# Optimization experiments

Hardware: AMD Instinct MI355X
Metric: run time of the kernel (lower is better)

The kernel has to match this reference:

```python
import jax, jax.numpy as jnp
import numpy as np

BETA = 0.25
CODEBOOK_SIZE = 1024
EMBED_DIM = 256


def setup_inputs() -> dict:
    key = jax.random.key(0)
    k1, k2 = jax.random.split(key)
    z_e = jax.random.normal(k1, (32, EMBED_DIM, 32, 32), dtype=jnp.float32)
    lim = 1.0 / CODEBOOK_SIZE
    emb_weight = jax.random.uniform(k2, (CODEBOOK_SIZE, EMBED_DIM),
                                    dtype=jnp.float32, minval=-lim, maxval=lim)
    return {"z_e": z_e, "emb_weight": emb_weight}


def reference(z_e, emb_weight):
    B, D, Gh, Gw = z_e.shape
    # (B, D, Gh, Gw) -> (N, D), N = B*Gh*Gw
    z_flat = jnp.transpose(z_e, (0, 2, 3, 1)).reshape(-1, D)

    # squared distances via ||z||^2 + ||e||^2 - 2 z.e
    z2 = jnp.sum(z_flat * z_flat, axis=1, keepdims=True)          # (N, 1)
    e2 = jnp.sum(emb_weight * emb_weight, axis=1)[None, :]        # (1, K)
    ze = jnp.einsum('nd,kd->nk', z_flat, emb_weight)              # (N, K)
    dist = z2 + e2 - 2.0 * ze

    idx_flat = jnp.argmin(dist, axis=1)                            # (N,)
    z_q_flat = emb_weight[idx_flat]                                # (N, D)

    sg = jax.lax.stop_gradient
    codebook_loss = jnp.mean((z_q_flat - sg(z_flat)) ** 2)
    commit_loss = jnp.mean((z_flat - sg(z_q_flat)) ** 2)
    vq_loss = codebook_loss + BETA * commit_loss

    # straight-through estimator
    z_q_st_flat = z_flat + sg(z_q_flat - z_flat)

    z_q_st = jnp.transpose(z_q_st_flat.reshape(B, Gh, Gw, D), (0, 3, 1, 2))
    idx = idx_flat.reshape(B, Gh, Gw)
    return z_q_st, idx, vq_loss
```

## Files before the change

### kernel.cpp

```cpp
#include <hip/hip_runtime.h>
#include <hip/hip_fp16.h>

#define MARGIN 6e-4f
#define RCAP 48

typedef __attribute__((ext_vector_type(8))) _Float16 half8;
typedef __attribute__((ext_vector_type(4))) float f32x4;

__device__ __forceinline__ unsigned short f2h(float x) {
    __half h = __float2half(x);
    return *reinterpret_cast<unsigned short*>(&h);
}
__device__ __forceinline__ void gload16(const void* g, void* l) {
    __builtin_amdgcn_global_load_lds(
        (const __attribute__((address_space(1))) void*)g,
        (__attribute__((address_space(3))) void*)l, 16, 0, 0);
}

__global__ __launch_bounds__(256) void k_prep_e(const float* __restrict__ e,
                                                float* __restrict__ e2,
                                                unsigned short* __restrict__ eh,
                                                int* __restrict__ rowCnt,
                                                float* __restrict__ lossAcc,
                                                int* __restrict__ doneCnt) {
    const int bi = blockIdx.x;
    const int t  = threadIdx.x;
    if (bi < 4) {
        int k = bi * 256 + t;
        const float4* p = (const float4*)(e + (size_t)k * 256);
        float s = 0.f;
#pragma unroll 4
        for (int c = 0; c < 64; ++c) {
            float4 v = p[c];
            s = fmaf(v.x, v.x, s); s = fmaf(v.y, v.y, s);
            s = fmaf(v.z, v.z, s); s = fmaf(v.w, v.w, s);
        }
        e2[k] = s;
    } else {
        int bb = bi - 4;
        int k0 = bb * 64;
#pragma unroll 4
        for (int i = 0; i < 16; ++i) {
            int flat = i * 256 + t;
            int row = flat >> 6, ch = flat & 63;
            int slab = ch >> 4, s8p = (ch >> 1) & 7, half = ch & 1;
            int s8 = s8p ^ (row & 7);
            int d  = slab * 64 + s8 * 8 + half * 4;
            float4 v = *(const float4*)(e + (size_t)(k0 + row) * 256 + d);
            uint2 ph = { (unsigned)f2h(v.x) | ((unsigned)f2h(v.y) << 16),
                         (unsigned)f2h(v.z) | ((unsigned)f2h(v.w) << 16) };
            size_t off = (size_t)(k0 + row) * 256 + slab * 64 + s8p * 8 + half * 4;
            *(uint2*)(eh + off) = ph;
        }
        if (bb == 0 && t == 0) { lossAcc[0] = 0.f; doneCnt[0] = 0; }
#pragma unroll
        for (int j = 0; j < 8; ++j)
            rowCnt[bb * 2048 + j * 256 + t] = 0;
    }
}

__global__ __launch_bounds__(512) void k_score(
        const float* __restrict__ z,
        const unsigned short* __restrict__ eh,
        const float* __restrict__ e2,
        float* __restrict__ z2,
        int* __restrict__ rowCnt, uint2* __restrict__ rowCand) {
    __shared__ unsigned short lds[32768];
    float* tile = (float*)&lds[16384];

    const int t    = threadIdx.x;
    const int lane = t & 63;
    const int w    = t >> 6;
    const int wr   = w >> 1;
    const int wc   = w & 1;
    const int c    = lane & 15;
    const int kq   = lane >> 4;
    const int n0   = blockIdx.x * 64;
    const int b    = n0 >> 10;
    const int nl0  = n0 & 1023;

    {
        float zs = 0.f;
        const int prow = t & 63;
        const int uu0  = (t >> 6) * 4;
        for (int ch = 0; ch < 4; ++ch) {
            const int d0 = ch * 64;
            __syncthreads();
#pragma unroll
            for (int i = 0; i < 2; ++i) {
                int flat = i * 512 + t;
                int dd = flat >> 4, q = flat & 15;
                float4 v = *(const float4*)(z + (size_t)b * 262144 +
                                            (size_t)(d0 + dd) * 1024 + nl0 + q * 4);
                int j0 = q * 4, sx = dd & 31;
                tile[dd * 64 + ((j0 + 0) ^ sx)] = v.x;
                tile[dd * 64 + ((j0 + 1) ^ sx)] = v.y;
                tile[dd * 64 + ((j0 + 2) ^ sx)] = v.z;
                tile[dd * 64 + ((j0 + 3) ^ sx)] = v.w;
            }
            __syncthreads();
            if (t < 64) {
#pragma unroll 16
                for (int dd = 0; dd < 64; ++dd) {
                    float v = tile[dd * 64 + (t ^ (dd & 31))];
                    zs = fmaf(v, v, zs);
                }
            }
#pragma unroll
            for (int u = uu0; u < uu0 + 4; ++u) {
                int dlo = u * 2;
                float a0 = tile[dlo * 64 + (prow ^ (dlo & 31))];
                float a1 = tile[(dlo + 1) * 64 + (prow ^ ((dlo + 1) & 31))];
                unsigned int pk = (unsigned)f2h(a0) | ((unsigned)f2h(a1) << 16);
                int g = u >> 2, w32 = u & 3;
                *(unsigned int*)&lds[prow * 256 + d0 +
                                     ((g ^ (prow & 7)) * 8) + w32 * 2] = pk;
            }
        }
        __syncthreads();
        if (t < 64) z2[n0 + t] = zs;
    }

#define STAGE_B(S, BUF)                                                      \
    do {                                                                     \
        int kc_ = (S) >> 2, dg_ = (S) & 3;                                   \
        _Pragma("unroll")                                                    \
        for (int p = 0; p < 2; ++p) {                                        \
            int slot = p * 512 + t;                                          \
            int code = slot >> 3, sg = slot & 7;                             \
            gload16(eh + (size_t)(kc_ * 128 + code) * 256 + dg_ * 64 + sg * 8, \
                    &lds[16384 + (BUF) * 8192 + (p * 512 + w * 64) * 8]);    \
        }                                                                    \
    } while (0)

    f32x4 acc[4];
#pragma unroll
    for (int cf = 0; cf < 4; ++cf) acc[cf] = (f32x4){0.f, 0.f, 0.f, 0.f};
    float m_run[4] = { 3.4e38f, 3.4e38f, 3.4e38f, 3.4e38f };

    const int rl = wr * 16 + c;
    STAGE_B(0, 0);
    __syncthreads();

    for (int s = 0; s < 32; ++s) {
        if (s < 31) STAGE_B(s + 1, (s + 1) & 1);
        {
            const int dg = s & 3;
            const unsigned short* Bb = &lds[16384 + (s & 1) * 8192];
#pragma unroll
            for (int ks = 0; ks < 2; ++ks) {
                int wo = ks * 4 + kq;
                half8 a = *(const half8*)&lds[rl * 256 + dg * 64 +
                                              (wo ^ (rl & 7)) * 8];
                half8 bfr[4];
#pragma unroll
                for (int cf = 0; cf < 4; ++cf) {
                    int cl = wc * 64 + cf * 16 + c;
                    bfr[cf] = *(const half8*)&Bb[cl * 64 + (wo ^ (cl & 7)) * 8];
                }
#pragma unroll
                for (int cf = 0; cf < 4; ++cf)
                    acc[cf] = __builtin_amdgcn_mfma_f32_16x16x32_f16(
                        a, bfr[cf], acc[cf], 0, 0, 0);
            }
        }
        if ((s & 3) == 3) {
            const int kc = s >> 2;
            float e2r[4];
#pragma unroll
            for (int cf = 0; cf < 4; ++cf)
                e2r[cf] = e2[kc * 128 + wc * 64 + cf * 16 + c];
            float mnew[4];
#pragma unroll
            for (int reg = 0; reg < 4; ++reg) {
                float mm = 3.4e38f;
#pragma unroll
                for (int cf = 0; cf < 4; ++cf)
                    mm = fminf(mm, fmaf(-2.f, acc[cf][reg], e2r[cf]));
                mnew[reg] = mm;
            }
#pragma unroll
            for (int m = 1; m < 16; m <<= 1)
#pragma unroll
                for (int reg = 0; reg < 4; ++reg)
                    mnew[reg] = fminf(mnew[reg], __shfl_xor(mnew[reg], m, 64));
#pragma unroll
            for (int reg = 0; reg < 4; ++reg)
                mnew[reg] = fminf(mnew[reg], m_run[reg]);
#pragma unroll
            for (int cf = 0; cf < 4; ++cf)
#pragma unroll
                for (int reg = 0; reg < 4; ++reg) {
                    float sv = fmaf(-2.f, acc[cf][reg], e2r[cf]);
                    if (sv <= mnew[reg] + MARGIN) {
                        int n = n0 + wr * 16 + kq * 4 + reg;
                        int k = kc * 128 + wc * 64 + cf * 16 + c;
                        int pos = atomicAdd(&rowCnt[n], 1);
                        if (pos < RCAP) {
                            uint2 cd; cd.x = (unsigned)k;
                            cd.y = __float_as_uint(sv);
                            rowCand[n * RCAP + pos] = cd;
                        }
                    }
                }
#pragma unroll
            for (int reg = 0; reg < 4; ++reg) m_run[reg] = mnew[reg];
#pragma unroll
            for (int cf = 0; cf < 4; ++cf) acc[cf] = (f32x4){0.f, 0.f, 0.f, 0.f};
        }
        __syncthreads();
    }
#undef STAGE_B
}

__global__ __launch_bounds__(256) void k_select(
        const float* __restrict__ z, const float* __restrict__ e,
        const float* __restrict__ z2a, const float* __restrict__ e2,
        const int* __restrict__ rowCnt, const uint2* __restrict__ rowCand,
        float* __restrict__ outIdx, int* __restrict__ wsIdx) {
    __shared__ float zstage[4][256];
    const int t = threadIdx.x, lane = t & 63, w = t >> 6;
    const int wid = blockIdx.x * 4 + w;
    for (int rr = 0; rr < 8; ++rr) {
        const int n = wid * 8 + rr;
        const int cnt = rowCnt[n];
        const float* zrow = z + (size_t)(n >> 10) * 262144 + (n & 1023);
        unsigned long long key = 0xFFFFFFFFFFFFFFFFULL;
        if (cnt <= RCAP) {
            float s = 3.4e38f;
            int   k = 0;
            if (lane < cnt) {
                uint2 cd = rowCand[n * RCAP + lane];
                k = (int)cd.x;
                s = __uint_as_float(cd.y);
            }
            float gmin = s;
#pragma unroll
            for (int m = 1; m < 64; m <<= 1)
                gmin = fminf(gmin, __shfl_xor(gmin, m, 64));
            bool surv = (lane < cnt) && (s <= gmin + MARGIN);
            unsigned long long bal = __ballot(surv);
            if (__popcll(bal) == 1) {
                if (surv) { outIdx[n] = (float)k; wsIdx[n] = k; }
                continue;
            }
#pragma unroll
            for (int j = 0; j < 4; ++j)
                zstage[w][lane + 64 * j] = zrow[(size_t)(lane + 64 * j) * 1024];
            if (surv) {
                const float* er = e + (size_t)k * 256;
                float ze = 0.f;
#pragma unroll 8
                for (int d = 0; d < 256; ++d)
                    ze = fmaf(zstage[w][d], er[d], ze);
                float t1 = z2a[n] + e2[k];
                float dist = fmaf(-2.f, ze, t1);
                key = ((unsigned long long)__float_as_uint(dist) << 32) |
                      (unsigned int)k;
            }
        } else {
#pragma unroll
            for (int j = 0; j < 4; ++j)
                zstage[w][lane + 64 * j] = zrow[(size_t)(lane + 64 * j) * 1024];
            const float z2r = z2a[n];
            for (int j = 0; j < 16; ++j) {
                int k = lane * 16 + j;
                const float* er = e + (size_t)k * 256;
                float ze = 0.f;
#pragma unroll 8
                for (int d = 0; d < 256; ++d)
                    ze = fmaf(zstage[w][d], er[d], ze);
                float t1 = z2r + e2[k];
                float dist = fmaf(-2.f, ze, t1);
                unsigned long long kk =
                    ((unsigned long long)__float_as_uint(dist) << 32) |
                    (unsigned int)k;
                if (kk < key) key = kk;
            }
        }
#pragma unroll
        for (int m = 1; m < 64; m <<= 1) {
            unsigned long long o = __shfl_xor(key, m, 64);
            if (o < key) key = o;
        }
        if (lane == 0) {
            int k = (int)(unsigned int)(key & 0xFFFFFFFFULL);
            outIdx[n] = (float)k;
            wsIdx[n]  = k;
        }
    }
}

__global__ __launch_bounds__(256) void k_epilogue(const float* __restrict__ z,
                                                  const float* __restrict__ e,
                                                  const int* __restrict__ wsIdx,
                                                  float* __restrict__ outZ,
                                                  float* __restrict__ lossAcc,
                                                  int* __restrict__ doneCnt,
                                                  float* __restrict__ outLoss) {
    __shared__ float zqT[8][1024];
    __shared__ int idxL[1024];
    __shared__ float wsum[4];
    const int t  = threadIdx.x;
    const int b  = blockIdx.x >> 5;
    const int dg = blockIdx.x & 31;
    const size_t zb = (size_t)b * 262144 + (size_t)(dg * 8) * 1024;

    float4 zreg[8];
#pragma unroll
    for (int i = 0; i < 8; ++i) {
        int flat = i * 256 + t;
        int dl = flat >> 8, q = flat & 255;
        zreg[i] = *(const float4*)(z + zb + (size_t)dl * 1024 + q * 4);
    }

#pragma unroll
    for (int c = 0; c < 4; ++c)
        idxL[c * 256 + t] = wsIdx[b * 1024 + c * 256 + t];
    __syncthreads();

#pragma unroll
    for (int c = 0; c < 4; ++c) {
        int nl = c * 256 + t;
        const float* er = e + (size_t)idxL[nl] * 256 + dg * 8;
        float4 v0 = *(const float4*)er;
        float4 v1 = *(const float4*)(er + 4);
        zqT[0][nl] = v0.x; zqT[1][nl] = v0.y;
        zqT[2][nl] = v0.z; zqT[3][nl] = v0.w;
        zqT[4][nl] = v1.x; zqT[5][nl] = v1.y;
        zqT[6][nl] = v1.z; zqT[7][nl] = v1.w;
    }
    __syncthreads();

    float s = 0.f;
#pragma unroll
    for (int i = 0; i < 8; ++i) {
        int flat = i * 256 + t;
        int dl = flat >> 8, q = flat & 255;
        float4 z4 = zreg[i];
        float4 q4 = *(const float4*)&zqT[dl][q * 4];
        float4 o; float df;
        df = q4.x - z4.x; s = fmaf(df, df, s); o.x = z4.x + df;
        df = q4.y - z4.y; s = fmaf(df, df, s); o.y = z4.y + df;
        df = q4.z - z4.z; s = fmaf(df, df, s); o.z = z4.z + df;
        df = q4.w - z4.w; s = fmaf(df, df, s); o.w = z4.w + df;
        *(float4*)(outZ + zb + (size_t)dl * 1024 + q * 4) = o;
    }

#pragma unroll
    for (int off = 32; off > 0; off >>= 1) s += __shfl_down(s, off, 64);
    if ((t & 63) == 0) wsum[t >> 6] = s;
    __syncthreads();
    if (t == 0) {
        float bs = ((wsum[0] + wsum[1]) + wsum[2]) + wsum[3];
        atomicAdd(lossAcc, bs);
        __threadfence();
        int tk = atomicAdd(doneCnt, 1);
        if (tk == 1023) {
            float L = atomicAdd(lossAcc, 0.0f);
            float m = L * (1.0f / 8388608.0f);
            outLoss[0] = m + 0.25f * m;
        }
    }
}

extern "C" void kernel_launch(void* const* d_in, const int* in_sizes, int n_in,
                              void* d_out, int out_size, void* d_ws, size_t ws_size,
                              hipStream_t stream) {
    const float* z = (const float*)d_in[0];
    const float* e = (const float*)d_in[1];
    float* out     = (float*)d_out;
    float* outIdx  = out + 8388608;
    float* outLoss = out + 8421376;

    float* z2      = (float*)d_ws;
    float* e2      = z2 + 32768;
    float* lossAcc = e2 + 1024;
    int*   doneCnt = (int*)(lossAcc + 64);
    int*   rowCnt  = doneCnt + 64;
    int*   wsIdx   = rowCnt + 32768;
    uintptr_t p = (uintptr_t)(wsIdx + 32768);
    p = (p + 255) & ~(uintptr_t)255;
    uint2* rowCand = (uint2*)p;
    unsigned short* eh = (unsigned short*)(rowCand + 32768 * RCAP);

    k_prep_e<<<20, 256, 0, stream>>>(e, e2, eh, rowCnt, lossAcc, doneCnt);
    k_score<<<512, 512, 0, stream>>>(z, eh, e2, z2, rowCnt, rowCand);
    k_select<<<1024, 256, 0, stream>>>(z, e, z2, e2, rowCnt, rowCand,
                                       outIdx, wsIdx);
    k_epilogue<<<1024, 256, 0, stream>>>(z, e, wsIdx, out, lossAcc,
                                         doneCnt, outLoss);
}
```

Baseline: 163.9 us.

## Fuse candidate selection into scoring kernel and restructure epilogue gather

Folds the k_select pass into the tail of k_score, so each block resolves the argmin for its own 64 rows right after scoring. This removes a kernel launch and the global round-trip of z2, and e2 and z2 are now kept in LDS. The epilogue is remapped to 512 blocks that gather codebook rows straight into registers (16 dims by 4 consecutive positions per thread) instead of staging through a transposed LDS tile. The cost is that selection now depends on same-block visibility of atomics and candidates (guarded by a fence and a barrier), and it runs at k_score's occupancy.

```diff
diff --git a/kernel.cpp b/kernel.cpp
--- a/kernel.cpp
+++ b/kernel.cpp
@@ -61,11 +61,15 @@
 
 __global__ __launch_bounds__(512) void k_score(
         const float* __restrict__ z,
+        const float* __restrict__ e,
         const unsigned short* __restrict__ eh,
         const float* __restrict__ e2,
-        float* __restrict__ z2,
-        int* __restrict__ rowCnt, uint2* __restrict__ rowCand) {
+        int* __restrict__ rowCnt, uint2* __restrict__ rowCand,
+        float* __restrict__ outIdx, int* __restrict__ wsIdx) {
     __shared__ unsigned short lds[32768];
+    __shared__ float e2L[1024];
+    __shared__ float z2L[64];
+
     float* tile = (float*)&lds[16384];
 
     const int t    = threadIdx.x;
@@ -79,6 +83,9 @@
     const int b    = n0 >> 10;
     const int nl0  = n0 & 1023;
 
+    e2L[t]       = e2[t];
+    e2L[t + 512] = e2[t + 512];
+
     {
         float zs = 0.f;
         const int prow = t & 63;
@@ -118,7 +125,7 @@
             }
         }
         __syncthreads();
-        if (t < 64) z2[n0 + t] = zs;
+        if (t < 64) z2L[t] = zs;
     }
 
 #define STAGE_B(S, BUF)                                                      \
@@ -169,7 +176,7 @@
             float e2r[4];
 #pragma unroll
             for (int cf = 0; cf < 4; ++cf)
-                e2r[cf] = e2[kc * 128 + wc * 64 + cf * 16 + c];
+                e2r[cf] = e2L[kc * 128 + wc * 64 + cf * 16 + c];
             float mnew[4];
 #pragma unroll
             for (int reg = 0; reg < 4; ++reg) {
@@ -211,82 +218,80 @@
         __syncthreads();
     }
 #undef STAGE_B
-}
-
-__global__ __launch_bounds__(256) void k_select(
-        const float* __restrict__ z, const float* __restrict__ e,
-        const float* __restrict__ z2a, const float* __restrict__ e2,
-        const int* __restrict__ rowCnt, const uint2* __restrict__ rowCand,
-        float* __restrict__ outIdx, int* __restrict__ wsIdx) {
-    __shared__ float zstage[4][256];
-    const int t = threadIdx.x, lane = t & 63, w = t >> 6;
-    const int wid = blockIdx.x * 4 + w;
-    for (int rr = 0; rr < 8; ++rr) {
-        const int n = wid * 8 + rr;
-        const int cnt = rowCnt[n];
-        const float* zrow = z + (size_t)(n >> 10) * 262144 + (n & 1023);
-        unsigned long long key = 0xFFFFFFFFFFFFFFFFULL;
-        if (cnt <= RCAP) {
-            float s = 3.4e38f;
-            int   k = 0;
-            if (lane < cnt) {
-                uint2 cd = rowCand[n * RCAP + lane];
-                k = (int)cd.x;
-                s = __uint_as_float(cd.y);
-            }
-            float gmin = s;
-#pragma unroll
-            for (int m = 1; m < 64; m <<= 1)
-                gmin = fminf(gmin, __shfl_xor(gmin, m, 64));
-            bool surv = (lane < cnt) && (s <= gmin + MARGIN);
-            unsigned long long bal = __ballot(surv);
-            if (__popcll(bal) == 1) {
-                if (surv) { outIdx[n] = (float)k; wsIdx[n] = k; }
-                continue;
-            }
-#pragma unroll
-            for (int j = 0; j < 4; ++j)
-                zstage[w][lane + 64 * j] = zrow[(size_t)(lane + 64 * j) * 1024];
-            if (surv) {
-                const float* er = e + (size_t)k * 256;
-                float ze = 0.f;
+
+    asm volatile("s_waitcnt vmcnt(0)" ::: "memory");
+    __threadfence();
+    __syncthreads();
+    {
+        float* zst = (float*)&lds[16384 + w * 512];
+        for (int rr = 0; rr < 8; ++rr) {
+            const int n = n0 + w * 8 + rr;
+            const int rloc = w * 8 + rr;
+            const int cnt = rowCnt[n];
+            const float* zrow = z + (size_t)b * 262144 + (n & 1023);
+            unsigned long long key = 0xFFFFFFFFFFFFFFFFULL;
+            if (cnt <= RCAP) {
+                float sc = 3.4e38f;
+                int   k = 0;
+                if (lane < cnt) {
+                    uint2 cd = rowCand[n * RCAP + lane];
+                    k = (int)cd.x;
+                    sc = __uint_as_float(cd.y);
+                }
+                float gmin = sc;
+#pragma unroll
+                for (int m = 1; m < 64; m <<= 1)
+                    gmin = fminf(gmin, __shfl_xor(gmin, m, 64));
+                bool surv = (lane < cnt) && (sc <= gmin + MARGIN);
+                unsigned long long bal = __ballot(surv);
+                if (__popcll(bal) == 1) {
+                    if (surv) { outIdx[n] = (float)k; wsIdx[n] = k; }
+                    continue;
+                }
+#pragma unroll
+                for (int j = 0; j < 4; ++j)
+                    zst[lane + 64 * j] = zrow[(size_t)(lane + 64 * j) * 1024];
+                if (surv) {
+                    const float* erk = e + (size_t)k * 256;
+                    float ze = 0.f;
 #pragma unroll 8
-                for (int d = 0; d < 256; ++d)
-                    ze = fmaf(zstage[w][d], er[d], ze);
-                float t1 = z2a[n] + e2[k];
-                float dist = fmaf(-2.f, ze, t1);
-                key = ((unsigned long long)__float_as_uint(dist) << 32) |
-                      (unsigned int)k;
-            }
-        } else {
-#pragma unroll
-            for (int j = 0; j < 4; ++j)
-                zstage[w][lane + 64 * j] = zrow[(size_t)(lane + 64 * j) * 1024];
-            const float z2r = z2a[n];
-            for (int j = 0; j < 16; ++j) {
-                int k = lane * 16 + j;
-                const float* er = e + (size_t)k * 256;
-                float ze = 0.f;
+                    for (int d = 0; d < 256; ++d)
+                        ze = fmaf(zst[d], erk[d], ze);
+                    float t1 = z2L[rloc] + e2L[k];
+                    float dist = fmaf(-2.f, ze, t1);
+                    key = ((unsigned long long)__float_as_uint(dist) << 32) |
+                          (unsigned int)k;
+                }
+            } else {
+#pragma unroll
+                for (int j = 0; j < 4; ++j)
+                    zst[lane + 64 * j] = zrow[(size_t)(lane + 64 * j) * 1024];
+                const float z2r = z2L[rloc];
+                for (int j = 0; j < 16; ++j) {
+                    int k = lane * 16 + j;
+                    const float* erk = e + (size_t)k * 256;
+                    float ze = 0.f;
 #pragma unroll 8
-                for (int d = 0; d < 256; ++d)
-                    ze = fmaf(zstage[w][d], er[d], ze);
-                float t1 = z2r + e2[k];
-                float dist = fmaf(-2.f, ze, t1);
-                unsigned long long kk =
-                    ((unsigned long long)__float_as_uint(dist) << 32) |
-                    (unsigned int)k;
-                if (kk < key) key = kk;
-            }
-        }
-#pragma unroll
-        for (int m = 1; m < 64; m <<= 1) {
-            unsigned long long o = __shfl_xor(key, m, 64);
-            if (o < key) key = o;
-        }
-        if (lane == 0) {
-            int k = (int)(unsigned int)(key & 0xFFFFFFFFULL);
-            outIdx[n] = (float)k;
-            wsIdx[n]  = k;
+                    for (int d = 0; d < 256; ++d)
+                        ze = fmaf(zst[d], erk[d], ze);
+                    float t1 = z2r + e2L[k];
+                    float dist = fmaf(-2.f, ze, t1);
+                    unsigned long long kk =
+                        ((unsigned long long)__float_as_uint(dist) << 32) |
+                        (unsigned int)k;
+                    if (kk < key) key = kk;
+                }
+            }
+#pragma unroll
+            for (int m = 1; m < 64; m <<= 1) {
+                unsigned long long o = __shfl_xor(key, m, 64);
+                if (o < key) key = o;
+            }
+            if (lane == 0) {
+                int k = (int)(unsigned int)(key & 0xFFFFFFFFULL);
+                outIdx[n] = (float)k;
+                wsIdx[n]  = k;
+            }
         }
     }
 }
@@ -298,53 +303,38 @@
                                                   float* __restrict__ lossAcc,
                                                   int* __restrict__ doneCnt,
                                                   float* __restrict__ outLoss) {
-    __shared__ float zqT[8][1024];
-    __shared__ int idxL[1024];
     __shared__ float wsum[4];
     const int t  = threadIdx.x;
-    const int b  = blockIdx.x >> 5;
-    const int dg = blockIdx.x & 31;
-    const size_t zb = (size_t)b * 262144 + (size_t)(dg * 8) * 1024;
-
-    float4 zreg[8];
-#pragma unroll
-    for (int i = 0; i < 8; ++i) {
-        int flat = i * 256 + t;
-        int dl = flat >> 8, q = flat & 255;
-        zreg[i] = *(const float4*)(z + zb + (size_t)dl * 1024 + q * 4);
-    }
-
-#pragma unroll
-    for (int c = 0; c < 4; ++c)
-        idxL[c * 256 + t] = wsIdx[b * 1024 + c * 256 + t];
-    __syncthreads();
-
-#pragma unroll
-    for (int c = 0; c < 4; ++c) {
-        int nl = c * 256 + t;
-        const float* er = e + (size_t)idxL[nl] * 256 + dg * 8;
-        float4 v0 = *(const float4*)er;
-        float4 v1 = *(const float4*)(er + 4);
-        zqT[0][nl] = v0.x; zqT[1][nl] = v0.y;
-        zqT[2][nl] = v0.z; zqT[3][nl] = v0.w;
-        zqT[4][nl] = v1.x; zqT[5][nl] = v1.y;
-        zqT[6][nl] = v1.z; zqT[7][nl] = v1.w;
-    }
-    __syncthreads();
+    const int b  = blockIdx.x >> 4;
+    const int d0 = (blockIdx.x & 15) * 16;
+    const int nl = t * 4;
+    const size_t zb = (size_t)b * 262144;
+
+    int4 idx4 = *(const int4*)&wsIdx[b * 1024 + nl];
+    float ev[4][16];
+    const int rows[4] = { idx4.x, idx4.y, idx4.z, idx4.w };
+#pragma unroll
+    for (int j = 0; j < 4; ++j) {
+        const float* er = e + (size_t)rows[j] * 256 + d0;
+#pragma unroll
+        for (int q = 0; q < 4; ++q) {
+            float4 v = *(const float4*)(er + q * 4);
+            ev[j][q * 4 + 0] = v.x; ev[j][q * 4 + 1] = v.y;
+            ev[j][q * 4 + 2] = v.z; ev[j][q * 4 + 3] = v.w;
+        }
+    }
 
     float s = 0.f;
 #pragma unroll
-    for (int i = 0; i < 8; ++i) {
-        int flat = i * 256 + t;
-        int dl = flat >> 8, q = flat & 255;
-        float4 z4 = zreg[i];
-        float4 q4 = *(const float4*)&zqT[dl][q * 4];
+    for (int dd = 0; dd < 16; ++dd) {
+        size_t go = zb + (size_t)(d0 + dd) * 1024 + nl;
+        float4 z4 = *(const float4*)(z + go);
         float4 o; float df;
-        df = q4.x - z4.x; s = fmaf(df, df, s); o.x = z4.x + df;
-        df = q4.y - z4.y; s = fmaf(df, df, s); o.y = z4.y + df;
-        df = q4.z - z4.z; s = fmaf(df, df, s); o.z = z4.z + df;
-        df = q4.w - z4.w; s = fmaf(df, df, s); o.w = z4.w + df;
-        *(float4*)(outZ + zb + (size_t)dl * 1024 + q * 4) = o;
+        df = ev[0][dd] - z4.x; s = fmaf(df, df, s); o.x = z4.x + df;
+        df = ev[1][dd] - z4.y; s = fmaf(df, df, s); o.y = z4.y + df;
+        df = ev[2][dd] - z4.z; s = fmaf(df, df, s); o.z = z4.z + df;
+        df = ev[3][dd] - z4.w; s = fmaf(df, df, s); o.w = z4.w + df;
+        *(float4*)(outZ + go) = o;
     }
 
 #pragma unroll
@@ -356,7 +346,7 @@
         atomicAdd(lossAcc, bs);
         __threadfence();
         int tk = atomicAdd(doneCnt, 1);
-        if (tk == 1023) {
+        if (tk == 511) {
             float L = atomicAdd(lossAcc, 0.0f);
             float m = L * (1.0f / 8388608.0f);
             outLoss[0] = m + 0.25f * m;
@@ -373,8 +363,7 @@
     float* outIdx  = out + 8388608;
     float* outLoss = out + 8421376;
 
-    float* z2      = (float*)d_ws;
-    float* e2      = z2 + 32768;
+    float* e2      = (float*)d_ws;
     float* lossAcc = e2 + 1024;
     int*   doneCnt = (int*)(lossAcc + 64);
     int*   rowCnt  = doneCnt + 64;
@@ -385,9 +374,8 @@
     unsigned short* eh = (unsigned short*)(rowCand + 32768 * RCAP);
 
     k_prep_e<<<20, 256, 0, stream>>>(e, e2, eh, rowCnt, lossAcc, doneCnt);
-    k_score<<<512, 512, 0, stream>>>(z, eh, e2, z2, rowCnt, rowCand);
-    k_select<<<1024, 256, 0, stream>>>(z, e, z2, e2, rowCnt, rowCand,
-                                       outIdx, wsIdx);
-    k_epilogue<<<1024, 256, 0, stream>>>(z, e, wsIdx, out, lossAcc,
-                                         doneCnt, outLoss);
-}
+    k_score<<<512, 512, 0, stream>>>(z, e, eh, e2, rowCnt, rowCand,
+                                     outIdx, wsIdx);
+    k_epilogue<<<512, 256, 0, stream>>>(z, e, wsIdx, out, lossAcc,
+                                        doneCnt, outLoss);
+}
```

New measurement: 221.8 us. +35.3%, slower.
